# Kernel tuning notes

Measured on AMD Instinct MI355X. Metric: run time of the kernel, lower is better.

## Reference

```python
import jax, jax.numpy as jnp
import numpy as np

EPS = 1e-5
BN_GAMMA = 1.0
BN_BETA = 1e-4  # per torch init: BN weight=1, bias=0.0001


def bn(h):
    # BatchNorm1d in training mode: biased batch variance
    mu = h.mean(axis=0)
    var = h.var(axis=0)
    return (h - mu) * (BN_GAMMA / jnp.sqrt(var + EPS)) + BN_BETA


def gcn_conv(h, W, b, row, col, n, edge_weight=None):
    # PyG-style GCNConv: linear -> add self loops (w=1) -> sym deg norm -> scatter-sum
    h = h @ W
    e = row.shape[0]
    ew = jnp.ones((e,), h.dtype) if edge_weight is None else edge_weight
    loop = jnp.arange(n, dtype=row.dtype)
    r = jnp.concatenate([row, loop])
    c = jnp.concatenate([col, loop])
    w = jnp.concatenate([ew, jnp.ones((n,), h.dtype)])
    deg = jax.ops.segment_sum(w, r, num_segments=n)
    dinv = jnp.where(deg > 0, jax.lax.rsqrt(deg + jnp.where(deg > 0, 0.0, 1.0)), 0.0)
    norm = dinv[r] * w * dinv[c]  # [E+N]
    msg = h[r] * norm[:, None]    # gather + per-edge scale
    out = jax.ops.segment_sum(msg, c, num_segments=n)  # scatter-aggregate
    return out + b


def readout(h, W1, b1, W2, b2):
    h = bn(h) @ W1 + b1
    h = bn(jax.nn.relu(h)) @ W2 + b2
    return jax.nn.log_softmax(h, axis=-1)


def setup_inputs() -> dict:
    key = jax.random.key(0)
    ks = jax.random.split(key, 12)
    N, E, F, H, C = 50000, 800000, 128, 128, 10
    s = 0.05
    return {
        "x": jax.random.normal(ks[0], (N, F), jnp.float32),
        "edge_index": jax.random.randint(ks[1], (2, E), 0, N, jnp.int32),
        "perm": jax.random.permutation(ks[2], N).astype(jnp.int32),
        "W_feat": jax.random.normal(ks[3], (F, H), jnp.float32) * s,
        "b_feat": jnp.zeros((H,), jnp.float32),
        "W_convs": jax.random.normal(ks[4], (3, H, H), jnp.float32) * s,
        "b_convs": jnp.zeros((3, H), jnp.float32),
        "W_ea": jax.random.normal(ks[5], (2 * H, 2), jnp.float32) * s,
        "b_ea": jnp.zeros((2,), jnp.float32),
        "W_na": jax.random.normal(ks[6], (H, 2), jnp.float32) * s,
        "b_na": jnp.zeros((2,), jnp.float32),
        "W_ctx": jax.random.normal(ks[7], (H, H), jnp.float32) * s,
        "b_ctx": jnp.zeros((H,), jnp.float32),
        "W_obj": jax.random.normal(ks[8], (H, H), jnp.float32) * s,
        "b_obj": jnp.zeros((H,), jnp.float32),
        "W_fc1": jax.random.normal(ks[9], (3, H, H), jnp.float32) * s,  # c,o,co
        "b_fc1": jnp.zeros((3, H), jnp.float32),
        "W_fc2": jax.random.normal(ks[10], (3, H, C), jnp.float32) * s,
        "b_fc2": jnp.zeros((3, C), jnp.float32),
    }


def reference(x, edge_index, perm, W_feat, b_feat, W_convs, b_convs, W_ea, b_ea,
              W_na, b_na, W_ctx, b_ctx, W_obj, b_obj, W_fc1, b_fc1, W_fc2, b_fc2):
    n = x.shape[0]
    row, col = edge_index[0], edge_index[1]
    h = bn(x)
    h = jax.nn.relu(h @ W_feat + b_feat)  # conv_feat has gfn=True -> pure linear
    for i in range(3):
        h = jax.nn.relu(gcn_conv(bn(h), W_convs[i], b_convs[i], row, col, n))
    edge_rep = jnp.concatenate([h[row], h[col]], axis=-1)  # [E, 2H]
    edge_att = jax.nn.softmax(edge_rep @ W_ea + b_ea, axis=-1)
    node_att = jax.nn.softmax(h @ W_na + b_na, axis=-1)
    xc = node_att[:, 0:1] * h
    xo = node_att[:, 1:2] * h
    xc = jax.nn.relu(gcn_conv(bn(xc), W_ctx, b_ctx, row, col, n, edge_att[:, 0]))
    xo = jax.nn.relu(gcn_conv(bn(xo), W_obj, b_obj, row, col, n, edge_att[:, 1]))
    xc_logis = readout(xc, W_fc1[0], b_fc1[0], W_fc2[0], b_fc2[0])
    xo_logis = readout(xo, W_fc1[1], b_fc1[1], W_fc2[1], b_fc2[1])
    xco_logis = readout(xc[perm] + xo, W_fc1[2], b_fc1[2], W_fc2[2], b_fc2[2])
    return (xc_logis, xo_logis, xco_logis)
```

## Files before the change

### kernel.cpp

```cpp
#include <hip/hip_runtime.h>
#include <math.h>

#define H 128
#define NCLS 10
#define EPS 1e-5f
#define BN_BETA 1e-4f
#define CS_BLOCKS 256
#define CPAD 16

typedef unsigned short u16;
typedef unsigned int u32;
typedef __attribute__((ext_vector_type(8))) short short8;
typedef __attribute__((ext_vector_type(4))) float floatx4;

__device__ inline float bflo(u32 u) { union { u32 i; float f; } a; a.i = u << 16; return a.f; }
__device__ inline float bfhi(u32 u) { union { u32 i; float f; } a; a.i = u & 0xffff0000u; return a.f; }
__device__ inline u16 f2bf(float f) {
  union { float f; u32 i; } v; v.f = f;
  return (u16)((v.i + 0x7fff + ((v.i >> 16) & 1)) >> 16);
}
__device__ inline u32 pack2(float a, float b) { return (u32)f2bf(a) | ((u32)f2bf(b) << 16); }

__device__ inline void reduce_partials(const float* __restrict__ P, int nb, int stride,
                                       int off0, int f, float* su_out, float* sq_out) {
  float su[8] = {0, 0, 0, 0, 0, 0, 0, 0}, sq[8] = {0, 0, 0, 0, 0, 0, 0, 0};
  int b = 0;
  for (; b + 8 <= nb; b += 8) {
#pragma unroll
    for (int u = 0; u < 8; u++) {
      const float* p = P + (size_t)(b + u) * stride + off0;
      su[u] += p[f];
      sq[u] += p[128 + f];
    }
  }
  for (; b < nb; b++) {
    const float* p = P + (size_t)b * stride + off0;
    su[0] += p[f];
    sq[0] += p[128 + f];
  }
  *su_out = ((su[0] + su[1]) + (su[2] + su[3])) + ((su[4] + su[5]) + (su[6] + su[7]));
  *sq_out = ((sq[0] + sq[1]) + (sq[2] + sq[3])) + ((sq[4] + sq[5]) + (sq[6] + sq[7]));
}

__device__ inline void fold256_body(const float* P, int nb, int stride, int off0,
                                    const float* W, const float* bias, float invN,
                                    int kp, u16* Wt, float* cf) {
  int f = threadIdx.x & 127;
  int half = threadIdx.x >> 7;
  int k = kp * 2 + half;
  float su, sq;
  reduce_partials(P, nb, stride, off0, f, &su, &sq);
  float mu = su * invN;
  float var = sq * invN - mu * mu;
  float s = 1.0f / sqrtf(fmaxf(var, 0.f) + EPS);
  float w = W[(size_t)f * H + k];
  Wt[(size_t)k * H + f] = f2bf(s * w);
  __shared__ float red[2][128];
  red[half][f] = (BN_BETA - mu * s) * w;
  __syncthreads();
  for (int o = 64; o > 0; o >>= 1) {
    if (f < o) red[half][f] += red[half][f + o];
    __syncthreads();
  }
  if (f == 0) cf[k] = red[half][0] + (bias ? bias[k] : 0.f);
}

__device__ inline void hist_body(const int* __restrict__ row, const int* __restrict__ col,
                                 int E, int* cnt_in_p, int* cnt_out_p,
                                 int* rank_in, int blk) {
  int e = blk * 256 + threadIdx.x;
  if (e < E) {
    rank_in[e] = atomicAdd(&cnt_in_p[(size_t)col[e] * CPAD], 1);
    atomicAdd(&cnt_out_p[(size_t)row[e] * CPAD], 1);
  }
}

__device__ inline void xstats_body(const float* __restrict__ x, int n4,
                                   float* __restrict__ stp, int blk) {
  int tid = threadIdx.x;
  int lane = tid & 63, wave = tid >> 6;
  float s[4] = {0, 0, 0, 0}, q[4] = {0, 0, 0, 0};
  int step = CS_BLOCKS * 256;
  for (int i = blk * 256 + tid; i < n4; i += step) {
    float4 v = ((const float4*)x)[i];
    s[0] += v.x; q[0] += v.x * v.x; s[1] += v.y; q[1] += v.y * v.y;
    s[2] += v.z; q[2] += v.z * v.z; s[3] += v.w; q[3] += v.w * v.w;
  }
#pragma unroll
  for (int k = 0; k < 4; k++) { s[k] += __shfl_xor(s[k], 32); q[k] += __shfl_xor(q[k], 32); }
  __shared__ float smx[4][256];
  int col = (lane & 31) * 4;
  if (lane < 32) {
#pragma unroll
    for (int k = 0; k < 4; k++) { smx[wave][col + k] = s[k]; smx[wave][128 + col + k] = q[k]; }
  }
  __syncthreads();
  stp[(size_t)blk * 256 + tid] = smx[0][tid] + smx[1][tid] + smx[2][tid] + smx[3][tid];
}

__device__ inline void scanA_body(const int* cnt_in_p, const int* cnt_out_p, int N,
                                  int* partial_in, float* dinv, int* degS, int blk) {
  int i = blk * 256 + threadIdx.x;
  int vo = (i < N) ? cnt_out_p[(size_t)i * CPAD] : 0;
  if (i < N) {
    dinv[i] = 1.0f / sqrtf((float)vo + 1.0f);
    degS[i] = vo;
  }
  __shared__ int sdA[256];
  sdA[threadIdx.x] = (i < N) ? cnt_in_p[(size_t)i * CPAD] : 0;
  __syncthreads();
  for (int o = 128; o > 0; o >>= 1) {
    if (threadIdx.x < o) sdA[threadIdx.x] += sdA[threadIdx.x + o];
    __syncthreads();
  }
  if (threadIdx.x == 0) partial_in[blk] = sdA[0];
}

__device__ inline void scanB1(const int* partial, int nb, int* blockoff) {
  __shared__ int sdB[256];
  int t = threadIdx.x;
  int v = (t < nb) ? partial[t] : 0;
  sdB[t] = v;
  __syncthreads();
  for (int o = 1; o < 256; o <<= 1) {
    int x = (t >= o) ? sdB[t - o] : 0;
    __syncthreads();
    sdB[t] += x;
    __syncthreads();
  }
  blockoff[t] = sdB[t] - v;
  __syncthreads();
}

__device__ inline void scanC1(const int* cnt_p, int N, const int* blockoff,
                              int* off, int E, int blk) {
  __shared__ int sdC[256];
  int t = threadIdx.x;
  int i = blk * 256 + t;
  int v = (i < N) ? cnt_p[(size_t)i * CPAD] : 0;
  sdC[t] = v;
  __syncthreads();
  for (int o = 1; o < 256; o <<= 1) {
    int x = (t >= o) ? sdC[t - o] : 0;
    __syncthreads();
    sdC[t] += x;
    __syncthreads();
  }
  if (i < N) off[i] = blockoff[blk] + sdC[t] - v;
  if (i == 0) off[N] = E;
  __syncthreads();
}

__device__ inline void place_body(const int* row, const int* col, int E,
                                  const int* rank_in, const int* off_in,
                                  const float* dinv, int* csr_src, int* slot_in,
                                  float* wn, int blk) {
  int e = blk * 256 + threadIdx.x;
  if (e < E) {
    int c = col[e], r = row[e];
    int si = off_in[c] + rank_in[e];
    csr_src[si] = r;
    slot_in[e] = si;
    wn[si] = dinv[r];
  }
}

__device__ inline void eatt_body(const int* row, const int* col, int E,
                                 const float2* p01, const float2* q01,
                                 const float* b_ea, const int* slot_in,
                                 float* att0s, float* degc, int blk) {
  int e = blk * 256 + threadIdx.x;
  if (e >= E) return;
  int r = row[e], c = col[e];
  float2 p = p01[r], q = q01[c];
  float l0 = p.x + q.x + b_ea[0];
  float l1 = p.y + q.y + b_ea[1];
  float a0 = 1.0f / (1.0f + expf(l1 - l0));
  att0s[slot_in[e]] = a0;
  atomicAdd(&degc[r], a0);
}

__device__ inline void xprestats_body(const u16* __restrict__ h,
                                      const float2* __restrict__ na01, int n4,
                                      float* __restrict__ stp, int blk) {
  int tid = threadIdx.x;
  int lane = tid & 63, wave = tid >> 6;
  float sc[4] = {0, 0, 0, 0}, qc[4] = {0, 0, 0, 0};
  float so[4] = {0, 0, 0, 0}, qo[4] = {0, 0, 0, 0};
  int step = CS_BLOCKS * 256;
  for (int i = blk * 256 + tid; i < n4; i += step) {
    int n = i >> 5;
    uint2 u = ((const uint2*)h)[i];
    float v0 = bflo(u.x), v1 = bfhi(u.x), v2 = bflo(u.y), v3 = bfhi(u.y);
    float2 ab = na01[n];
    float a = ab.x, b = ab.y;
    float c0 = v0 * a, c1 = v1 * a, c2 = v2 * a, c3 = v3 * a;
    float o0 = v0 * b, o1 = v1 * b, o2 = v2 * b, o3 = v3 * b;
    sc[0] += c0; qc[0] += c0 * c0; sc[1] += c1; qc[1] += c1 * c1;
    sc[2] += c2; qc[2] += c2 * c2; sc[3] += c3; qc[3] += c3 * c3;
    so[0] += o0; qo[0] += o0 * o0; so[1] += o1; qo[1] += o1 * o1;
    so[2] += o2; qo[2] += o2 * o2; so[3] += o3; qo[3] += o3 * o3;
  }
#pragma unroll
  for (int k = 0; k < 4; k++) {
    sc[k] += __shfl_xor(sc[k], 32); qc[k] += __shfl_xor(qc[k], 32);
    so[k] += __shfl_xor(so[k], 32); qo[k] += __shfl_xor(qo[k], 32);
  }
  __shared__ float smp[4][512];
  int col = (lane & 31) * 4;
  if (lane < 32) {
#pragma unroll
    for (int k = 0; k < 4; k++) {
      smp[wave][col + k] = sc[k];
      smp[wave][128 + col + k] = qc[k];
      smp[wave][256 + col + k] = so[k];
      smp[wave][384 + col + k] = qo[k];
    }
  }
  __syncthreads();
  float r0 = smp[0][tid] + smp[1][tid] + smp[2][tid] + smp[3][tid];
  float r1 = smp[0][256 + tid] + smp[1][256 + tid] + smp[2][256 + tid] + smp[3][256 + tid];
  stp[(size_t)blk * 512 + tid] = r0;
  stp[(size_t)blk * 512 + 256 + tid] = r1;
}

__device__ inline void gemm_core(const u16* A, const float* Afp, const u16* Bt,
                                 const float* cf, const float* b2, const float* sumw,
                                 u16* C, int N, int relu, int blk, float* stp) {
  int tid = threadIdx.x;
  int wave = tid >> 6, lane = tid & 63;
  int l15 = lane & 15, quad = lane >> 4;
  int row0 = (blk * 4 + wave) * 16;
  if (row0 >= N && !stp) return;
  int arow = row0 + l15;
  short8 a[4];
  short8 z8 = {0, 0, 0, 0, 0, 0, 0, 0};
  if (Afp) {
#pragma unroll
    for (int k4 = 0; k4 < 4; k4++) {
      if (arow < N) {
        const float* p = Afp + (size_t)arow * H + k4 * 32 + quad * 8;
        float4 f0 = *(const float4*)p;
        float4 f1 = *(const float4*)(p + 4);
        union { short8 s8; u32 u[4]; } cv;
        cv.u[0] = pack2(f0.x, f0.y); cv.u[1] = pack2(f0.z, f0.w);
        cv.u[2] = pack2(f1.x, f1.y); cv.u[3] = pack2(f1.z, f1.w);
        a[k4] = cv.s8;
      } else a[k4] = z8;
    }
  } else {
#pragma unroll
    for (int k4 = 0; k4 < 4; k4++)
      a[k4] = (arow < N) ? *(const short8*)(A + (size_t)arow * H + k4 * 32 + quad * 8) : z8;
  }
  float srow[4];
  if (sumw) {
#pragma unroll
    for (int r = 0; r < 4; r++) {
      int row = row0 + quad * 4 + r;
      srow[r] = (row < N) ? sumw[row] : 0.f;
    }
  }
  float ps[8], pq[8];
#pragma unroll
  for (int nt = 0; nt < 8; nt++) {
    floatx4 acc = {0.f, 0.f, 0.f, 0.f};
    const u16* bp = Bt + (size_t)(nt * 16 + l15) * H + quad * 8;
#pragma unroll
    for (int k4 = 0; k4 < 4; k4++) {
      short8 b = *(const short8*)(bp + k4 * 32);
      acc = __builtin_amdgcn_mfma_f32_16x16x32_bf16(a[k4], b, acc, 0, 0, 0);
    }
    int col = nt * 16 + l15;
    float base = cf[col];
    float bb = b2 ? b2[col] : 0.f;
    float s_ = 0.f, q_ = 0.f;
#pragma unroll
    for (int r = 0; r < 4; r++) {
      int row = row0 + quad * 4 + r;
      if (row < N) {
        float v = acc[r] + (sumw ? srow[r] * base + bb : base);
        if (relu) v = fmaxf(v, 0.f);
        s_ += v; q_ += v * v;
        C[(size_t)row * H + col] = f2bf(v);
      }
    }
    ps[nt] = s_; pq[nt] = q_;
  }
  if (stp) {
    __shared__ float sred[4][256];
#pragma unroll
    for (int nt = 0; nt < 8; nt++) {
      ps[nt] += __shfl_xor(ps[nt], 16); ps[nt] += __shfl_xor(ps[nt], 32);
      pq[nt] += __shfl_xor(pq[nt], 16); pq[nt] += __shfl_xor(pq[nt], 32);
    }
    if (quad == 0) {
#pragma unroll
      for (int nt = 0; nt < 8; nt++) {
        sred[wave][nt * 16 + l15] = ps[nt];
        sred[wave][128 + nt * 16 + l15] = pq[nt];
      }
    }
    __syncthreads();
    stp[(size_t)blk * 256 + tid] =
        sred[0][tid] + sred[1][tid] + sred[2][tid] + sred[3][tid];
  }
}

__global__ __launch_bounds__(256) void hist_xstats_kernel(
    const int* row, const int* col, int E, int* cnt_in_p, int* cnt_out_p,
    int* rank_in, int gE, const float* x, int n4, float* stpX) {
  if ((int)blockIdx.x < gE)
    hist_body(row, col, E, cnt_in_p, cnt_out_p, rank_in, blockIdx.x);
  else
    xstats_body(x, n4, stpX, blockIdx.x - gE);
}

__global__ __launch_bounds__(256) void scanA_fold_kernel(
    const int* cnt_in_p, const int* cnt_out_p, int N, int* partial_in,
    float* dinv, int* degS, int SB, const float* stpX, const float* W_feat,
    const float* b_feat, float invN, u16* WtA, float* cfA) {
  if ((int)blockIdx.x < SB)
    scanA_body(cnt_in_p, cnt_out_p, N, partial_in, dinv, degS, blockIdx.x);
  else
    fold256_body(stpX, CS_BLOCKS, 256, 0, W_feat, b_feat, invN, blockIdx.x - SB, WtA, cfA);
}

__global__ __launch_bounds__(256) void scanB_gemmx_kernel(
    const int* partial_in, int nb, int* blockoff_in,
    const float* x, const u16* WtA, const float* cfA, u16* C,
    int N, float* stpG) {
  if (blockIdx.x == 0) {
    scanB1(partial_in, nb, blockoff_in);
  } else {
    gemm_core(nullptr, x, WtA, cfA, nullptr, nullptr, C, N, 1, blockIdx.x - 1, stpG);
  }
}

__global__ __launch_bounds__(256) void scanC_fold_kernel(
    const int* cnt_in_p, int N, const int* blockoff_in, int* off_in, int E, int SB,
    const float* stpG, int nbG, const float* Wc, float invN, u16* WtB, float* cfB) {
  if ((int)blockIdx.x < SB) {
    scanC1(cnt_in_p, N, blockoff_in, off_in, E, blockIdx.x);
  } else {
    fold256_body(stpG, nbG, 256, 0, Wc, nullptr, invN, blockIdx.x - SB, WtB, cfB);
  }
}

__global__ __launch_bounds__(256) void place_gemm_kernel(
    const int* row, const int* col, int E, const int* rank_in,
    const int* off_in, const float* dinv, int* csr_src,
    int* slot_in, float* wn, int gE,
    const u16* A, const u16* WtB, const float* cfB, u16* C, int N) {
  if ((int)blockIdx.x < gE)
    place_body(row, col, E, rank_in, off_in, dinv, csr_src, slot_in, wn, blockIdx.x);
  else
    gemm_core(A, nullptr, WtB, cfB, nullptr, nullptr, C, N, 0, blockIdx.x - gE, nullptr);
}

__global__ __launch_bounds__(256) void eatt_xpre_kernel(
    const int* row, const int* col, int E, const float2* p01, const float2* q01,
    const float* b_ea, const int* slot_in, float* att0s, float* degc,
    int gE, const u16* h, const float2* na01, int n4, float* stpPre) {
  if ((int)blockIdx.x < gE)
    eatt_body(row, col, E, p01, q01, b_ea, slot_in, att0s, degc, blockIdx.x);
  else
    xprestats_body(h, na01, n4, stpPre, blockIdx.x - gE);
}

__global__ __launch_bounds__(256) void fold2_kernel(
    const float* stpPre, const float* W_ctx, const float* W_obj, float invN,
    u16* Wt2, float* cf2) {
  int b = blockIdx.x;
  int j = b >> 6, kp = b & 63;
  fold256_body(stpPre, CS_BLOCKS, 512, j * 256, j ? W_obj : W_ctx, nullptr, invN, kp,
               Wt2 + (size_t)j * H * H, cf2 + j * H);
}

__global__ __launch_bounds__(256) void permadd_fold31_kernel(
    const u16* xc, const u16* xo, const int* perm, u16* outb, int n4, float* stpCO,
    const float* stpG, int nbG, const float* W_fc1, const float* b_fc1, float invN,
    u16* Wt3, float* cf3) {
  int tid = threadIdx.x;
  if ((int)blockIdx.x >= CS_BLOCKS) {
    int b = blockIdx.x - CS_BLOCKS;
    int j = b >> 6, kp = b & 63;
    fold256_body(stpG + (size_t)j * nbG * 256, nbG, 256, 0, W_fc1 + (size_t)j * H * H,
                 b_fc1 + j * H, invN, kp, Wt3 + (size_t)j * H * H, cf3 + j * H);
    return;
  }
  int blk = blockIdx.x;
  int lane = tid & 63, wave = tid >> 6;
  float s[4] = {0, 0, 0, 0}, q[4] = {0, 0, 0, 0};
  int step = CS_BLOCKS * 256;
  for (int i = blk * 256 + tid; i < n4; i += step) {
    int n = i >> 5, k = i & 31;
    int p = perm[n];
    uint2 a = ((const uint2*)xc)[(size_t)p * 32 + k];
    uint2 b = ((const uint2*)xo)[i];
    float f0 = bflo(a.x) + bflo(b.x), f1 = bfhi(a.x) + bfhi(b.x);
    float f2 = bflo(a.y) + bflo(b.y), f3 = bfhi(a.y) + bfhi(b.y);
    ((uint2*)outb)[i] = make_uint2(pack2(f0, f1), pack2(f2, f3));
    s[0] += f0; q[0] += f0 * f0; s[1] += f1; q[1] += f1 * f1;
    s[2] += f2; q[2] += f2 * f2; s[3] += f3; q[3] += f3 * f3;
  }
#pragma unroll
  for (int k = 0; k < 4; k++) { s[k] += __shfl_xor(s[k], 32); q[k] += __shfl_xor(q[k], 32); }
  __shared__ float smq[4][256];
  int col = (lane & 31) * 4;
  if (lane < 32) {
#pragma unroll
    for (int k = 0; k < 4; k++) { smq[wave][col + k] = s[k]; smq[wave][128 + col + k] = q[k]; }
  }
  __syncthreads();
  stpCO[(size_t)blk * 256 + tid] = smq[0][tid] + smq[1][tid] + smq[2][tid] + smq[3][tid];
}

__global__ __launch_bounds__(256) void fold256_kernel(
    const float* P, int nb, const float* W, const float* bias, float invN,
    u16* Wt, float* cf) {
  fold256_body(P, nb, 256, 0, W, bias, invN, blockIdx.x, Wt, cf);
}

__global__ __launch_bounds__(128) void fold10x3_kernel(
    const float* stpZ, int nb, const float* W_fc2, const float* b_fc2, float invN,
    float* W2f, float* c2f) {
  int j = blockIdx.x / NCLS, k = blockIdx.x % NCLS;
  const float* P = stpZ + (size_t)j * nb * 256;
  int f = threadIdx.x;
  float su, sq;
  reduce_partials(P, nb, 256, 0, f, &su, &sq);
  float mu = su * invN;
  float var = sq * invN - mu * mu;
  float s = 1.0f / sqrtf(fmaxf(var, 0.f) + EPS);
  float w = W_fc2[(size_t)j * H * NCLS + (size_t)f * NCLS + k];
  W2f[(size_t)j * H * NCLS + (size_t)f * NCLS + k] = s * w;
  __shared__ float red1[H];
  red1[f] = (BN_BETA - mu * s) * w;
  __syncthreads();
  for (int o = 64; o > 0; o >>= 1) {
    if (f < o) red1[f] += red1[f + o];
    __syncthreads();
  }
  if (f == 0) c2f[j * 16 + k] = red1[0] + b_fc2[j * NCLS + k];
}

__global__ __launch_bounds__(256) void gemm_kernel(
    const u16* A, const u16* Bt, const float* cf, u16* C, int N, int relu) {
  gemm_core(A, nullptr, Bt, cf, nullptr, nullptr, C, N, relu, blockIdx.x, nullptr);
}

__global__ __launch_bounds__(256) void gemm2sw_kernel(
    u16* B0, u16* B1, const u16* Wt2, const float* cf2,
    const float* b0, const float* b1, const float* sw0, const float* sw1,
    int N, int gG, float* stp) {
  int j = blockIdx.x / gG, blk = blockIdx.x % gG;
  u16* Z = j ? B1 : B0;
  gemm_core(Z, nullptr, Wt2 + (size_t)j * H * H, cf2 + j * H, j ? b1 : b0,
            j ? sw1 : sw0, Z, N, 1, blk, stp + (size_t)j * gG * 256);
}

__global__ __launch_bounds__(256) void gemm3_kernel(
    u16* Z0, u16* Z1, u16* Z2, const u16* Wt3, const float* cf3,
    int N, int gG, float* stp) {
  int j = blockIdx.x / gG, blk = blockIdx.x % gG;
  u16* Z = (j == 0) ? Z0 : (j == 1) ? Z1 : Z2;
  gemm_core(Z, nullptr, Wt3 + (size_t)j * H * H, cf3 + j * H, nullptr, nullptr,
            Z, N, 1, blk, stp + (size_t)j * gG * 256);
}

__global__ __launch_bounds__(256) void colstats_kernel(
    const u16* __restrict__ X, int N, float* __restrict__ stp) {
  int tid = threadIdx.x;
  int li = tid & 15, rg = tid >> 4;
  int wave = tid >> 6, lane = tid & 63;
  const uint4* T = (const uint4*)X;
  float s[8] = {0, 0, 0, 0, 0, 0, 0, 0}, q[8] = {0, 0, 0, 0, 0, 0, 0, 0};
  for (int r = blockIdx.x * 16 + rg; r < N; r += CS_BLOCKS * 16) {
    uint4 u = T[(size_t)r * 16 + li];
    float f[8] = {bflo(u.x), bfhi(u.x), bflo(u.y), bfhi(u.y),
                  bflo(u.z), bfhi(u.z), bflo(u.w), bfhi(u.w)};
#pragma unroll
    for (int j = 0; j < 8; j++) { s[j] += f[j]; q[j] += f[j] * f[j]; }
  }
#pragma unroll
  for (int j = 0; j < 8; j++) {
    s[j] += __shfl_xor(s[j], 16); s[j] += __shfl_xor(s[j], 32);
    q[j] += __shfl_xor(q[j], 16); q[j] += __shfl_xor(q[j], 32);
  }
  __shared__ float smc[4][256];
  if ((lane & 48) == 0) {
#pragma unroll
    for (int j = 0; j < 8; j++) {
      smc[wave][li * 8 + j] = s[j];
      smc[wave][128 + li * 8 + j] = q[j];
    }
  }
  __syncthreads();
  stp[(size_t)blockIdx.x * 256 + tid] = smc[0][tid] + smc[1][tid] + smc[2][tid] + smc[3][tid];
}

#define ACC8(A, U, W)                                             \
  A[0] += (W) * bflo(U.x); A[1] += (W) * bfhi(U.x);               \
  A[2] += (W) * bflo(U.y); A[3] += (W) * bfhi(U.y);               \
  A[4] += (W) * bflo(U.z); A[5] += (W) * bfhi(U.z);               \
  A[6] += (W) * bflo(U.w); A[7] += (W) * bfhi(U.w);

__global__ __launch_bounds__(256) void agg_kernel(
    const u16* __restrict__ t, const int* __restrict__ csr_src,
    const float* __restrict__ wseg, const int* __restrict__ off,
    const float* __restrict__ dinv, const float* __restrict__ bias,
    u16* __restrict__ out, int N) {
  int v = blockIdx.x * 4 + (threadIdx.x >> 6);
  if (v >= N) return;
  int lane = threadIdx.x & 63;
  int g = lane >> 4, li = lane & 15;
  const uint4* T = (const uint4*)t;
  float dv = dinv[v];
  float acc[8] = {0.f, 0.f, 0.f, 0.f, 0.f, 0.f, 0.f, 0.f};
  if (g == 0) {
    uint4 u = T[(size_t)v * 16 + li];
    float w0 = dv * dv;
    ACC8(acc, u, w0)
  }
  int s0 = off[v], s1 = off[v + 1];
  for (int s = s0; s < s1; s += 32) {
    int ix[8]; float wv[8];
#pragma unroll
    for (int u = 0; u < 8; u++) {
      int e = s + g + u * 4;
      bool ok = e < s1;
      int e2 = ok ? e : s0;
      ix[u] = csr_src[e2];
      wv[u] = ok ? wseg[e2] : 0.f;
    }
    uint4 uu[8];
#pragma unroll
    for (int u = 0; u < 8; u++) uu[u] = T[(size_t)ix[u] * 16 + li];
#pragma unroll
    for (int u = 0; u < 8; u++) { float w = wv[u] * dv; ACC8(acc, uu[u], w) }
  }
#pragma unroll
  for (int j = 0; j < 8; j++) {
    acc[j] += __shfl_xor(acc[j], 16);
    acc[j] += __shfl_xor(acc[j], 32);
  }
  if (g == 0) {
    float o[8];
#pragma unroll
    for (int j = 0; j < 8; j++) o[j] = fmaxf(acc[j] + bias[li * 8 + j], 0.f);
    uint4 w4;
    w4.x = pack2(o[0], o[1]); w4.y = pack2(o[2], o[3]);
    w4.z = pack2(o[4], o[5]); w4.w = pack2(o[6], o[7]);
    ((uint4*)out)[(size_t)v * 16 + li] = w4;
  }
}

__global__ __launch_bounds__(256) void aggdual_kernel(
    const u16* __restrict__ h, const int* __restrict__ csr_src,
    const float* __restrict__ att0s, const int* __restrict__ degS,
    const float* __restrict__ degc, const float2* __restrict__ na01,
    const int* __restrict__ off,
    u16* __restrict__ gc, u16* __restrict__ go,
    float* __restrict__ sumw_c, float* __restrict__ sumw_o, int N) {
  int v = blockIdx.x * 4 + (threadIdx.x >> 6);
  if (v >= N) return;
  int lane = threadIdx.x & 63;
  int g = lane >> 4, li = lane & 15;
  const uint4* T = (const uint4*)h;
  float dgc = degc[v];
  float dvc = 1.0f / sqrtf(dgc + 1.0f);
  float dvo = 1.0f / sqrtf((float)degS[v] - dgc + 1.0f);
  float ac[8] = {0.f, 0.f, 0.f, 0.f, 0.f, 0.f, 0.f, 0.f};
  float ao[8] = {0.f, 0.f, 0.f, 0.f, 0.f, 0.f, 0.f, 0.f};
  float swc = 0.f, swo = 0.f;
  if (g == 0) {
    uint4 u = T[(size_t)v * 16 + li];
    float2 na = na01[v];
    float wc = dvc * dvc, wo = dvo * dvo;
    float wch = wc * na.x, woh = wo * na.y;
    ACC8(ac, u, wch)
    ACC8(ao, u, woh)
  }
  int s0 = off[v], s1 = off[v + 1];
  for (int s = s0; s < s1; s += 16) {
    int ix[4]; float a0v[4];
#pragma unroll
    for (int u = 0; u < 4; u++) {
      int e = s + g + u * 4;
      bool ok = e < s1;
      int e2 = ok ? e : s0;
      ix[u] = csr_src[e2];
      a0v[u] = ok ? att0s[e2] : 0.f;
      if (!ok) a0v[u] = -1.f;
    }
    uint4 uu[4];
    float2 nav[4];
    float dS[4], dC[4];
#pragma unroll
    for (int u = 0; u < 4; u++) {
      int sidx = ix[u];
      uu[u] = T[(size_t)sidx * 16 + li];
      nav[u] = na01[sidx];
      dS[u] = (float)degS[sidx];
      dC[u] = degc[sidx];
    }
#pragma unroll
    for (int u = 0; u < 4; u++) {
      float a0 = a0v[u];
      bool ok = a0 >= 0.f;
      float r0 = ok ? a0 / sqrtf(dC[u] + 1.0f) : 0.f;
      float r1 = ok ? (1.0f - a0) / sqrtf(dS[u] - dC[u] + 1.0f) : 0.f;
      float wc = r0 * nav[u].x * dvc; ACC8(ac, uu[u], wc)
      float wo = r1 * nav[u].y * dvo; ACC8(ao, uu[u], wo)
      swc += r0; swo += r1;
    }
  }
#pragma unroll
  for (int j = 0; j < 8; j++) {
    ac[j] += __shfl_xor(ac[j], 16); ac[j] += __shfl_xor(ac[j], 32);
    ao[j] += __shfl_xor(ao[j], 16); ao[j] += __shfl_xor(ao[j], 32);
  }
  swc += __shfl_xor(swc, 16); swc += __shfl_xor(swc, 32);
  swo += __shfl_xor(swo, 16); swo += __shfl_xor(swo, 32);
  if (g == 0) {
    uint4 wc4, wo4;
    wc4.x = pack2(ac[0], ac[1]); wc4.y = pack2(ac[2], ac[3]);
    wc4.z = pack2(ac[4], ac[5]); wc4.w = pack2(ac[6], ac[7]);
    wo4.x = pack2(ao[0], ao[1]); wo4.y = pack2(ao[2], ao[3]);
    wo4.z = pack2(ao[4], ao[5]); wo4.w = pack2(ao[6], ao[7]);
    ((uint4*)gc)[(size_t)v * 16 + li] = wc4;
    ((uint4*)go)[(size_t)v * 16 + li] = wo4;
    if (li == 0) {
      sumw_c[v] = dvc * swc + dvc * dvc;
      sumw_o[v] = dvo * swo + dvo * dvo;
    }
  }
}

__global__ __launch_bounds__(256) void natt_kernel(
    const u16* __restrict__ h, int N,
    const float* __restrict__ W_na, const float* __restrict__ b_na,
    const float* __restrict__ W_ea,
    float2* __restrict__ na01, float2* __restrict__ p01, float2* __restrict__ q01) {
  int n = blockIdx.x * 256 + threadIdx.x;
  if (n >= N) return;
  float sa0 = 0, sa1 = 0, sp0 = 0, sp1 = 0, sq0 = 0, sq1 = 0;
  const uint2* hr = (const uint2*)(h + (size_t)n * H);
  for (int c = 0; c < 32; c++) {
    uint2 u = hr[c];
    float v0 = bflo(u.x), v1 = bfhi(u.x), v2 = bflo(u.y), v3 = bfhi(u.y);
    int k = c * 4;
    sa0 += v0 * W_na[k * 2] + v1 * W_na[k * 2 + 2] + v2 * W_na[k * 2 + 4] + v3 * W_na[k * 2 + 6];
    sa1 += v0 * W_na[k * 2 + 1] + v1 * W_na[k * 2 + 3] + v2 * W_na[k * 2 + 5] + v3 * W_na[k * 2 + 7];
    sp0 += v0 * W_ea[k * 2] + v1 * W_ea[k * 2 + 2] + v2 * W_ea[k * 2 + 4] + v3 * W_ea[k * 2 + 6];
    sp1 += v0 * W_ea[k * 2 + 1] + v1 * W_ea[k * 2 + 3] + v2 * W_ea[k * 2 + 5] + v3 * W_ea[k * 2 + 7];
    sq0 += v0 * W_ea[(H + k) * 2] + v1 * W_ea[(H + k) * 2 + 2] + v2 * W_ea[(H + k) * 2 + 4] + v3 * W_ea[(H + k) * 2 + 6];
    sq1 += v0 * W_ea[(H + k) * 2 + 1] + v1 * W_ea[(H + k) * 2 + 3] + v2 * W_ea[(H + k) * 2 + 5] + v3 * W_ea[(H + k) * 2 + 7];
  }
  sa0 += b_na[0]; sa1 += b_na[1];
  float m = fmaxf(sa0, sa1);
  float e0 = expf(sa0 - m), e1 = expf(sa1 - m);
  float inv = 1.f / (e0 + e1);
  na01[n] = make_float2(e0 * inv, e1 * inv);
  p01[n] = make_float2(sp0, sp1);
  q01[n] = make_float2(sq0, sq1);
}

__global__ __launch_bounds__(256) void fc2x3_kernel(
    const u16* __restrict__ z0, const u16* __restrict__ z1, const u16* __restrict__ z2,
    const float* __restrict__ W2f, const float* __restrict__ c2f,
    float* __restrict__ outp, int N, int gN) {
  int j = blockIdx.x / gN, blk = blockIdx.x % gN;
  int n = blk * 256 + threadIdx.x;
  if (n >= N) return;
  const u16* z = (j == 0) ? z0 : (j == 1) ? z1 : z2;
  const float* W2 = W2f + (size_t)j * H * NCLS;
  const float* c2 = c2f + j * 16;
  float* op = outp + (size_t)j * N * NCLS;
  float acc[NCLS];
#pragma unroll
  for (int c = 0; c < NCLS; c++) acc[c] = c2[c];
  const uint2* zr = (const uint2*)(z + (size_t)n * H);
  for (int c4 = 0; c4 < 32; c4++) {
    uint2 u = zr[c4];
    float v[4] = {bflo(u.x), bfhi(u.x), bflo(u.y), bfhi(u.y)};
    int k = c4 * 4;
#pragma unroll
    for (int jj = 0; jj < 4; jj++)
#pragma unroll
      for (int c = 0; c < NCLS; c++) acc[c] += v[jj] * W2[(k + jj) * NCLS + c];
  }
  float m = acc[0];
#pragma unroll
  for (int c = 1; c < NCLS; c++) m = fmaxf(m, acc[c]);
  float s = 0.f;
#pragma unroll
  for (int c = 0; c < NCLS; c++) s += expf(acc[c] - m);
  float lse = logf(s) + m;
#pragma unroll
  for (int c = 0; c < NCLS; c++) op[(size_t)n * NCLS + c] = acc[c] - lse;
}

extern "C" void kernel_launch(void* const* d_in, const int* in_sizes, int n_in,
                              void* d_out, int out_size, void* d_ws, size_t ws_size,
                              hipStream_t stream) {
  const int N = in_sizes[0] / H;
  const int E = in_sizes[1] / 2;
  const float* x = (const float*)d_in[0];
  const int* ei = (const int*)d_in[1];
  const int* row = ei;
  const int* col = ei + E;
  const int* perm = (const int*)d_in[2];
  const float* W_feat = (const float*)d_in[3];
  const float* b_feat = (const float*)d_in[4];
  const float* W_convs = (const float*)d_in[5];
  const float* b_convs = (const float*)d_in[6];
  const float* W_ea = (const float*)d_in[7];
  const float* b_ea = (const float*)d_in[8];
  const float* W_na = (const float*)d_in[9];
  const float* b_na = (const float*)d_in[10];
  const float* W_ctx = (const float*)d_in[11];
  const float* b_ctx = (const float*)d_in[12];
  const float* W_obj = (const float*)d_in[13];
  const float* b_obj = (const float*)d_in[14];
  const float* W_fc1 = (const float*)d_in[15];
  const float* b_fc1 = (const float*)d_in[16];
  const float* W_fc2 = (const float*)d_in[17];
  const float* b_fc2 = (const float*)d_in[18];
  float* out = (float*)d_out;

  const int gG = (N + 63) / 64;
  const int gN = (N + 255) / 256;
  const int gE = (E + 255) / 256;
  const int SB = (N + 255) / 256;
  const int n4 = N * 32;
  const int gAgg = (N + 3) / 4;
  const float invN = 1.0f / (float)N;

  char* base = (char*)d_ws;
  size_t off_b = 0;
  auto alloc = [&](size_t bytes) -> void* {
    void* p = base + off_b;
    off_b = (off_b + bytes + 255) & ~(size_t)255;
    return p;
  };
  size_t NB2 = (size_t)N * H * sizeof(u16);
  u16* bufA = (u16*)alloc(NB2);
  u16* bufB = (u16*)alloc(NB2);
  u16* bufC = (u16*)alloc(NB2);
  u16* bufD = (u16*)alloc(NB2);
  int* zeroblk = (int*)alloc(((size_t)2 * CPAD * N + N) * 4);
  int* cnt_in_p = zeroblk;
  int* cnt_out_p = zeroblk + (size_t)CPAD * N;
  float* degc = (float*)(zeroblk + (size_t)2 * CPAD * N);
  int* degS = (int*)alloc((size_t)N * 4);
  float* stpX = (float*)alloc((size_t)CS_BLOCKS * 256 * 4);
  float* stpG = (float*)alloc(3 * (size_t)gG * 256 * 4);
  float* stpPre = (float*)alloc((size_t)CS_BLOCKS * 512 * 4);
  float* stpCO = (float*)alloc((size_t)CS_BLOCKS * 256 * 4);
  int* off_in = (int*)alloc(((size_t)N + 1) * 4);
  float* dinv = (float*)alloc((size_t)N * 4);
  float* sumw_c = (float*)alloc((size_t)N * 4);
  float* sumw_o = (float*)alloc((size_t)N * 4);
  float2* na01 = (float2*)alloc((size_t)N * 8);
  float2* p01 = (float2*)alloc((size_t)N * 8);
  float2* q01 = (float2*)alloc((size_t)N * 8);
  int* partial_in = (int*)alloc(256 * 4);
  int* blockoff_in = (int*)alloc(256 * 4);
  u16* WtA = (u16*)alloc((size_t)H * H * 2);
  u16* WtB = (u16*)alloc((size_t)H * H * 2);
  u16* Wt2 = (u16*)alloc(2 * (size_t)H * H * 2);
  u16* Wt3 = (u16*)alloc(3 * (size_t)H * H * 2);
  float* cfA = (float*)alloc(H * 4);
  float* cfB = (float*)alloc(H * 4);
  float* cf2 = (float*)alloc(2 * H * 4);
  float* cf3 = (float*)alloc(3 * H * 4);
  float* W2f = (float*)alloc(3 * (size_t)H * NCLS * 4);
  float* c2f = (float*)alloc(3 * 16 * 4);
  int* rank_in = (int*)alloc((size_t)E * 4);
  int* csr_src = (int*)alloc((size_t)E * 4);
  int* slot_in = (int*)alloc((size_t)E * 4);
  float* att0s = (float*)alloc((size_t)E * 4);
  float* wn = (float*)alloc((size_t)E * 4);

  hipMemsetAsync(zeroblk, 0, ((size_t)2 * CPAD * N + N) * 4, stream);

  hist_xstats_kernel<<<gE + CS_BLOCKS, 256, 0, stream>>>(
      row, col, E, cnt_in_p, cnt_out_p, rank_in, gE, x, n4, stpX);
  scanA_fold_kernel<<<SB + 64, 256, 0, stream>>>(
      cnt_in_p, cnt_out_p, N, partial_in, dinv, degS, SB, stpX, W_feat, b_feat,
      invN, WtA, cfA);
  scanB_gemmx_kernel<<<1 + gG, 256, 0, stream>>>(
      partial_in, SB, blockoff_in, x, WtA, cfA, bufA, N, stpG);
  scanC_fold_kernel<<<SB + 64, 256, 0, stream>>>(
      cnt_in_p, N, blockoff_in, off_in, E, SB, stpG, gG, W_convs, invN, WtB, cfB);
  place_gemm_kernel<<<gE + gG, 256, 0, stream>>>(
      row, col, E, rank_in, off_in, dinv, csr_src, slot_in, wn, gE,
      bufA, WtB, cfB, bufB, N);
  agg_kernel<<<gAgg, 256, 0, stream>>>(bufB, csr_src, wn, off_in, dinv, b_convs, bufA, N);

  for (int i = 1; i < 3; ++i) {
    colstats_kernel<<<CS_BLOCKS, 256, 0, stream>>>(bufA, N, stpX);
    fold256_kernel<<<64, 256, 0, stream>>>(stpX, CS_BLOCKS, W_convs + (size_t)i * H * H,
                                           nullptr, invN, WtB, cfB);
    gemm_kernel<<<gG, 256, 0, stream>>>(bufA, WtB, cfB, bufB, N, 0);
    agg_kernel<<<gAgg, 256, 0, stream>>>(bufB, csr_src, wn, off_in, dinv,
                                         b_convs + (size_t)i * H, bufA, N);
  }

  natt_kernel<<<gN, 256, 0, stream>>>(bufA, N, W_na, b_na, W_ea, na01, p01, q01);
  eatt_xpre_kernel<<<gE + CS_BLOCKS, 256, 0, stream>>>(
      row, col, E, p01, q01, b_ea, slot_in, att0s, degc, gE,
      bufA, na01, n4, stpPre);
  fold2_kernel<<<128, 256, 0, stream>>>(stpPre, W_ctx, W_obj, invN, Wt2, cf2);
  aggdual_kernel<<<gAgg, 256, 0, stream>>>(bufA, csr_src, att0s, degS, degc, na01,
                                           off_in, bufC, bufD, sumw_c, sumw_o, N);
  gemm2sw_kernel<<<2 * gG, 256, 0, stream>>>(bufC, bufD, Wt2, cf2, b_ctx, b_obj,
                                             sumw_c, sumw_o, N, gG, stpG);

  permadd_fold31_kernel<<<CS_BLOCKS + 128, 256, 0, stream>>>(
      bufC, bufD, perm, bufA, n4, stpCO, stpG, gG, W_fc1, b_fc1, invN, Wt3, cf3);
  fold256_kernel<<<64, 256, 0, stream>>>(stpCO, CS_BLOCKS, W_fc1 + 2 * (size_t)H * H,
                                         b_fc1 + 2 * H, invN, Wt3 + 2 * (size_t)H * H,
                                         cf3 + 2 * H);
  gemm3_kernel<<<3 * gG, 256, 0, stream>>>(bufC, bufD, bufA, Wt3, cf3, N, gG, stpG);
  fold10x3_kernel<<<3 * NCLS, 128, 0, stream>>>(stpG, gG, W_fc2, b_fc2, invN, W2f, c2f);
  fc2x3_kernel<<<3 * gN, 256, 0, stream>>>(bufC, bufD, bufA, W2f, c2f, out, N, gN);
}
```

Before: 857.9 us.

## Replace global atomic out-degree and attention-degree sums with LDS-binned partial histograms

```diff
diff --git a/kernel.cpp b/kernel.cpp
--- a/kernel.cpp
+++ b/kernel.cpp
@@ -6,7 +6,8 @@
 #define EPS 1e-5f
 #define BN_BETA 1e-4f
 #define CS_BLOCKS 256
-#define CPAD 16
+#define ODC 32
+#define RNG_CAP 12544
 
 typedef unsigned short u16;
 typedef unsigned int u32;
@@ -65,18 +66,53 @@
   if (f == 0) cf[k] = red[half][0] + (bias ? bias[k] : 0.f);
 }
 
-__device__ inline void hist_body(const int* __restrict__ row, const int* __restrict__ col,
-                                 int E, int* cnt_in_p, int* cnt_out_p,
-                                 int* rank_in, int blk) {
+__device__ inline void hist_body(const int* __restrict__ col, int E,
+                                 int* cnt_in, int* rank_in, int blk) {
   int e = blk * 256 + threadIdx.x;
-  if (e < E) {
-    rank_in[e] = atomicAdd(&cnt_in_p[(size_t)col[e] * CPAD], 1);
-    atomicAdd(&cnt_out_p[(size_t)row[e] * CPAD], 1);
-  }
+  if (e < E) rank_in[e] = atomicAdd(&cnt_in[col[e]], 1);
+}
+
+__device__ inline void odpart_body(const int* __restrict__ row, int E, int N,
+                                   int* __restrict__ partialOD, int RNG, int CE,
+                                   int* bins, int blk) {
+  int c = blk % ODC, r = blk / ODC;
+  int lo = r * RNG;
+  int hi = lo + RNG; if (hi > N) hi = N;
+  int nb = hi - lo;
+  for (int i = threadIdx.x; i < nb; i += 256) bins[i] = 0;
+  __syncthreads();
+  int e0 = c * CE, e1 = e0 + CE; if (e1 > E) e1 = E;
+  for (int e = e0 + threadIdx.x; e < e1; e += 256) {
+    int rr = row[e];
+    if (rr >= lo && rr < hi) atomicAdd(&bins[rr - lo], 1);
+  }
+  __syncthreads();
+  int* dst = partialOD + (size_t)c * N + lo;
+  for (int i = threadIdx.x; i < nb; i += 256) dst[i] = bins[i];
+}
+
+__device__ inline void degcpart_body(const int* __restrict__ row,
+                                     const float* __restrict__ att_e, int E, int N,
+                                     float* __restrict__ partialDC, int RNG, int CE,
+                                     float* bins, int blk) {
+  int c = blk % ODC, r = blk / ODC;
+  int lo = r * RNG;
+  int hi = lo + RNG; if (hi > N) hi = N;
+  int nb = hi - lo;
+  for (int i = threadIdx.x; i < nb; i += 256) bins[i] = 0.f;
+  __syncthreads();
+  int e0 = c * CE, e1 = e0 + CE; if (e1 > E) e1 = E;
+  for (int e = e0 + threadIdx.x; e < e1; e += 256) {
+    int rr = row[e];
+    if (rr >= lo && rr < hi) atomicAdd(&bins[rr - lo], att_e[e]);
+  }
+  __syncthreads();
+  float* dst = partialDC + (size_t)c * N + lo;
+  for (int i = threadIdx.x; i < nb; i += 256) dst[i] = bins[i];
 }
 
 __device__ inline void xstats_body(const float* __restrict__ x, int n4,
-                                   float* __restrict__ stp, int blk) {
+                                   float* __restrict__ stp, int blk, float* smx) {
   int tid = threadIdx.x;
   int lane = tid & 63, wave = tid >> 6;
   float s[4] = {0, 0, 0, 0}, q[4] = {0, 0, 0, 0};
@@ -88,26 +124,31 @@
   }
 #pragma unroll
   for (int k = 0; k < 4; k++) { s[k] += __shfl_xor(s[k], 32); q[k] += __shfl_xor(q[k], 32); }
-  __shared__ float smx[4][256];
   int col = (lane & 31) * 4;
   if (lane < 32) {
 #pragma unroll
-    for (int k = 0; k < 4; k++) { smx[wave][col + k] = s[k]; smx[wave][128 + col + k] = q[k]; }
-  }
-  __syncthreads();
-  stp[(size_t)blk * 256 + tid] = smx[0][tid] + smx[1][tid] + smx[2][tid] + smx[3][tid];
-}
-
-__device__ inline void scanA_body(const int* cnt_in_p, const int* cnt_out_p, int N,
+    for (int k = 0; k < 4; k++) {
+      smx[wave * 256 + col + k] = s[k];
+      smx[wave * 256 + 128 + col + k] = q[k];
+    }
+  }
+  __syncthreads();
+  stp[(size_t)blk * 256 + tid] =
+      smx[tid] + smx[256 + tid] + smx[512 + tid] + smx[768 + tid];
+}
+
+__device__ inline void scanA_body(const int* cnt_in, const int* partialOD, int N,
                                   int* partial_in, float* dinv, int* degS, int blk) {
   int i = blk * 256 + threadIdx.x;
-  int vo = (i < N) ? cnt_out_p[(size_t)i * CPAD] : 0;
   if (i < N) {
+    int vo = 0;
+#pragma unroll 8
+    for (int c = 0; c < ODC; c++) vo += partialOD[(size_t)c * N + i];
     dinv[i] = 1.0f / sqrtf((float)vo + 1.0f);
     degS[i] = vo;
   }
   __shared__ int sdA[256];
-  sdA[threadIdx.x] = (i < N) ? cnt_in_p[(size_t)i * CPAD] : 0;
+  sdA[threadIdx.x] = (i < N) ? cnt_in[i] : 0;
   __syncthreads();
   for (int o = 128; o > 0; o >>= 1) {
     if (threadIdx.x < o) sdA[threadIdx.x] += sdA[threadIdx.x + o];
@@ -132,12 +173,12 @@
   __syncthreads();
 }
 
-__device__ inline void scanC1(const int* cnt_p, int N, const int* blockoff,
+__device__ inline void scanC1(const int* cnt, int N, const int* blockoff,
                               int* off, int E, int blk) {
   __shared__ int sdC[256];
   int t = threadIdx.x;
   int i = blk * 256 + t;
-  int v = (i < N) ? cnt_p[(size_t)i * CPAD] : 0;
+  int v = (i < N) ? cnt[i] : 0;
   sdC[t] = v;
   __syncthreads();
   for (int o = 1; o < 256; o <<= 1) {
@@ -168,7 +209,7 @@
 __device__ inline void eatt_body(const int* row, const int* col, int E,
                                  const float2* p01, const float2* q01,
                                  const float* b_ea, const int* slot_in,
-                                 float* att0s, float* degc, int blk) {
+                                 float* att0s, float* att_e, int blk) {
   int e = blk * 256 + threadIdx.x;
   if (e >= E) return;
   int r = row[e], c = col[e];
@@ -177,7 +218,7 @@
   float l1 = p.y + q.y + b_ea[1];
   float a0 = 1.0f / (1.0f + expf(l1 - l0));
   att0s[slot_in[e]] = a0;
-  atomicAdd(&degc[r], a0);
+  att_e[e] = a0;
 }
 
 __device__ inline void xprestats_body(const u16* __restrict__ h,
@@ -307,21 +348,26 @@
   }
 }
 
-__global__ __launch_bounds__(256) void hist_xstats_kernel(
-    const int* row, const int* col, int E, int* cnt_in_p, int* cnt_out_p,
-    int* rank_in, int gE, const float* x, int n4, float* stpX) {
-  if ((int)blockIdx.x < gE)
-    hist_body(row, col, E, cnt_in_p, cnt_out_p, rank_in, blockIdx.x);
+__global__ __launch_bounds__(256) void hist_od_xstats_kernel(
+    const int* row, const int* col, int E, int* cnt_in, int* rank_in, int gE,
+    int N, int* partialOD, int RNG, int CE, int gOD,
+    const float* x, int n4, float* stpX) {
+  __shared__ __align__(16) char smem[50176];
+  int b = blockIdx.x;
+  if (b < gE)
+    hist_body(col, E, cnt_in, rank_in, b);
+  else if (b < gE + gOD)
+    odpart_body(row, E, N, partialOD, RNG, CE, (int*)smem, b - gE);
   else
-    xstats_body(x, n4, stpX, blockIdx.x - gE);
+    xstats_body(x, n4, stpX, b - gE - gOD, (float*)smem);
 }
 
 __global__ __launch_bounds__(256) void scanA_fold_kernel(
-    const int* cnt_in_p, const int* cnt_out_p, int N, int* partial_in,
+    const int* cnt_in, const int* partialOD, int N, int* partial_in,
     float* dinv, int* degS, int SB, const float* stpX, const float* W_feat,
     const float* b_feat, float invN, u16* WtA, float* cfA) {
   if ((int)blockIdx.x < SB)
-    scanA_body(cnt_in_p, cnt_out_p, N, partial_in, dinv, degS, blockIdx.x);
+    scanA_body(cnt_in, partialOD, N, partial_in, dinv, degS, blockIdx.x);
   else
     fold256_body(stpX, CS_BLOCKS, 256, 0, W_feat, b_feat, invN, blockIdx.x - SB, WtA, cfA);
 }
@@ -338,10 +384,10 @@
 }
 
 __global__ __launch_bounds__(256) void scanC_fold_kernel(
-    const int* cnt_in_p, int N, const int* blockoff_in, int* off_in, int E, int SB,
+    const int* cnt_in, int N, const int* blockoff_in, int* off_in, int E, int SB,
     const float* stpG, int nbG, const float* Wc, float invN, u16* WtB, float* cfB) {
   if ((int)blockIdx.x < SB) {
-    scanC1(cnt_in_p, N, blockoff_in, off_in, E, blockIdx.x);
+    scanC1(cnt_in, N, blockoff_in, off_in, E, blockIdx.x);
   } else {
     fold256_body(stpG, nbG, 256, 0, Wc, nullptr, invN, blockIdx.x - SB, WtB, cfB);
   }
@@ -360,21 +406,38 @@
 
 __global__ __launch_bounds__(256) void eatt_xpre_kernel(
     const int* row, const int* col, int E, const float2* p01, const float2* q01,
-    const float* b_ea, const int* slot_in, float* att0s, float* degc,
+    const float* b_ea, const int* slot_in, float* att0s, float* att_e,
     int gE, const u16* h, const float2* na01, int n4, float* stpPre) {
   if ((int)blockIdx.x < gE)
-    eatt_body(row, col, E, p01, q01, b_ea, slot_in, att0s, degc, blockIdx.x);
+    eatt_body(row, col, E, p01, q01, b_ea, slot_in, att0s, att_e, blockIdx.x);
   else
     xprestats_body(h, na01, n4, stpPre, blockIdx.x - gE);
 }
 
-__global__ __launch_bounds__(256) void fold2_kernel(
+__global__ __launch_bounds__(256) void degcpart_fold2_kernel(
+    const int* row, const float* att_e, int E, int N, float* partialDC,
+    int RNG, int CE, int gDC,
     const float* stpPre, const float* W_ctx, const float* W_obj, float invN,
     u16* Wt2, float* cf2) {
-  int b = blockIdx.x;
-  int j = b >> 6, kp = b & 63;
-  fold256_body(stpPre, CS_BLOCKS, 512, j * 256, j ? W_obj : W_ctx, nullptr, invN, kp,
-               Wt2 + (size_t)j * H * H, cf2 + j * H);
+  __shared__ __align__(16) char smem[50176];
+  if ((int)blockIdx.x < gDC) {
+    degcpart_body(row, att_e, E, N, partialDC, RNG, CE, (float*)smem, blockIdx.x);
+  } else {
+    int b = blockIdx.x - gDC;
+    int j = b >> 6, kp = b & 63;
+    fold256_body(stpPre, CS_BLOCKS, 512, j * 256, j ? W_obj : W_ctx, nullptr, invN, kp,
+                 Wt2 + (size_t)j * H * H, cf2 + j * H);
+  }
+}
+
+__global__ __launch_bounds__(256) void degc_reduce_kernel(
+    const float* __restrict__ partialDC, float* __restrict__ degc, int N) {
+  int i = blockIdx.x * 256 + threadIdx.x;
+  if (i >= N) return;
+  float s = 0.f;
+#pragma unroll 8
+  for (int c = 0; c < ODC; c++) s += partialDC[(size_t)c * N + i];
+  degc[i] = s;
 }
 
 __global__ __launch_bounds__(256) void permadd_fold31_kernel(
@@ -738,6 +801,11 @@
   const int gAgg = (N + 3) / 4;
   const float invN = 1.0f / (float)N;
 
+  int R = (N + RNG_CAP - 1) / RNG_CAP; if (R < 1) R = 1;
+  const int RNG = (N + R - 1) / R;
+  const int CE = (E + ODC - 1) / ODC;
+  const int gOD = R * ODC;
+
   char* base = (char*)d_ws;
   size_t off_b = 0;
   auto alloc = [&](size_t bytes) -> void* {
@@ -750,11 +818,11 @@
   u16* bufB = (u16*)alloc(NB2);
   u16* bufC = (u16*)alloc(NB2);
   u16* bufD = (u16*)alloc(NB2);
-  int* zeroblk = (int*)alloc(((size_t)2 * CPAD * N + N) * 4);
-  int* cnt_in_p = zeroblk;
-  int* cnt_out_p = zeroblk + (size_t)CPAD * N;
-  float* degc = (float*)(zeroblk + (size_t)2 * CPAD * N);
+  int* cnt_in = (int*)alloc((size_t)N * 4);
+  float* degc = (float*)alloc((size_t)N * 4);
   int* degS = (int*)alloc((size_t)N * 4);
+  int* partialOD = (int*)alloc((size_t)ODC * N * 4);
+  float* partialDC = (float*)alloc((size_t)ODC * N * 4);
   float* stpX = (float*)alloc((size_t)CS_BLOCKS * 256 * 4);
   float* stpG = (float*)alloc(3 * (size_t)gG * 256 * 4);
   float* stpPre = (float*)alloc((size_t)CS_BLOCKS * 512 * 4);
@@ -782,19 +850,20 @@
   int* csr_src = (int*)alloc((size_t)E * 4);
   int* slot_in = (int*)alloc((size_t)E * 4);
   float* att0s = (float*)alloc((size_t)E * 4);
+  float* att_e = (float*)alloc((size_t)E * 4);
   float* wn = (float*)alloc((size_t)E * 4);
 
-  hipMemsetAsync(zeroblk, 0, ((size_t)2 * CPAD * N + N) * 4, stream);
-
-  hist_xstats_kernel<<<gE + CS_BLOCKS, 256, 0, stream>>>(
-      row, col, E, cnt_in_p, cnt_out_p, rank_in, gE, x, n4, stpX);
+  hipMemsetAsync(cnt_in, 0, (size_t)N * 4, stream);
+
+  hist_od_xstats_kernel<<<gE + gOD + CS_BLOCKS, 256, 0, stream>>>(
+      row, col, E, cnt_in, rank_in, gE, N, partialOD, RNG, CE, gOD, x, n4, stpX);
   scanA_fold_kernel<<<SB + 64, 256, 0, stream>>>(
-      cnt_in_p, cnt_out_p, N, partial_in, dinv, degS, SB, stpX, W_feat, b_feat,
+      cnt_in, partialOD, N, partial_in, dinv, degS, SB, stpX, W_feat, b_feat,
       invN, WtA, cfA);
   scanB_gemmx_kernel<<<1 + gG, 256, 0, stream>>>(
       partial_in, SB, blockoff_in, x, WtA, cfA, bufA, N, stpG);
   scanC_fold_kernel<<<SB + 64, 256, 0, stream>>>(
-      cnt_in_p, N, blockoff_in, off_in, E, SB, stpG, gG, W_convs, invN, WtB, cfB);
+      cnt_in, N, blockoff_in, off_in, E, SB, stpG, gG, W_convs, invN, WtB, cfB);
   place_gemm_kernel<<<gE + gG, 256, 0, stream>>>(
       row, col, E, rank_in, off_in, dinv, csr_src, slot_in, wn, gE,
       bufA, WtB, cfB, bufB, N);
@@ -811,9 +880,11 @@
 
   natt_kernel<<<gN, 256, 0, stream>>>(bufA, N, W_na, b_na, W_ea, na01, p01, q01);
   eatt_xpre_kernel<<<gE + CS_BLOCKS, 256, 0, stream>>>(
-      row, col, E, p01, q01, b_ea, slot_in, att0s, degc, gE,
+      row, col, E, p01, q01, b_ea, slot_in, att0s, att_e, gE,
       bufA, na01, n4, stpPre);
-  fold2_kernel<<<128, 256, 0, stream>>>(stpPre, W_ctx, W_obj, invN, Wt2, cf2);
+  degcpart_fold2_kernel<<<gOD + 128, 256, 0, stream>>>(
+      row, att_e, E, N, partialDC, RNG, CE, gOD, stpPre, W_ctx, W_obj, invN, Wt2, cf2);
+  degc_reduce_kernel<<<gN, 256, 0, stream>>>(partialDC, degc, N);
   aggdual_kernel<<<gAgg, 256, 0, stream>>>(bufA, csr_src, att0s, degS, degc, na01,
                                            off_in, bufC, bufD, sumw_c, sumw_o, N);
   gemm2sw_kernel<<<2 * gG, 256, 0, stream>>>(bufC, bufD, Wt2, cf2, b_ctx, b_obj,
```

Measured after the change: 858.9 us. About the same (+0.1%).
